# Kernel optimization log

Measured on AMD Instinct MI355X. Metric: run time of the kernel, lower is better.

## Reference

```python
import jax, jax.numpy as jnp
import numpy as np
import math

WINDOW = 512
N_HEAD = 16

def setup_inputs() -> dict:
    key = jax.random.key(0)
    ks = jax.random.split(key, 5)
    B, L, D = 2, 4096, 1024
    s = 0.02
    return {
        "x": jax.random.normal(ks[0], (B, L, D), dtype=jnp.float32),
        "Wq": jax.random.normal(ks[1], (D, D), dtype=jnp.float32) * s,
        "bq": jnp.zeros((D,), jnp.float32),
        "Wk": jax.random.normal(ks[2], (D, D), dtype=jnp.float32) * s,
        "bk": jnp.zeros((D,), jnp.float32),
        "Wv": jax.random.normal(ks[3], (D, D), dtype=jnp.float32) * s,
        "bv": jnp.zeros((D,), jnp.float32),
        "Wo": jax.random.normal(ks[4], (D, D), dtype=jnp.float32) * s,
        "bo": jnp.zeros((D,), jnp.float32),
    }

def reference(x, Wq, bq, Wk, bk, Wv, bv, Wo, bo):
    # Chunked sliding-window MHA (eval mode, dropout inactive).
    B, L, D = x.shape
    W, H = WINDOW, N_HEAD
    dh = D // H
    C = L // W  # number of query chunks
    scale = 1.0 / math.sqrt(dh)

    # Project full sequence once (linear, per-token -> identical math).
    q = x @ Wq.T + bq
    k = x @ Wk.T + bk
    v = x @ Wv.T + bv

    # Pad K/V by one window at the front so every chunk sees 2W keys.
    kp = jnp.pad(k, ((0, 0), (W, 0), (0, 0)))
    vp = jnp.pad(v, ((0, 0), (W, 0), (0, 0)))
    idx = jnp.arange(C)[:, None] * W + jnp.arange(2 * W)[None, :]  # [C, 2W] into padded seq
    kc = kp[:, idx].reshape(B, C, 2 * W, H, dh)
    vc = vp[:, idx].reshape(B, C, 2 * W, H, dh)
    qc = q.reshape(B, C, W, H, dh)

    scores = jnp.einsum('bcqhd,bckhd->bchqk', qc, kc) * scale  # [B,C,H,W,2W]
    valid = (idx >= W)  # padded positions (chunk 0's lookback) are invalid
    scores = jnp.where(valid[None, :, None, None, :], scores, jnp.float32(-1e9))
    attn = jax.nn.softmax(scores, axis=-1)
    out = jnp.einsum('bchqk,bckhd->bcqhd', attn, vc).reshape(B, L, D)
    return out @ Wo.T + bo
```

## Files before the change

kernel.cpp:

```cpp
#include <hip/hip_runtime.h>
#include <hip/hip_bf16.h>

typedef __hip_bfloat16 bf16;
typedef __attribute__((ext_vector_type(8))) short bf16x8;
typedef __attribute__((ext_vector_type(4))) float f32x4;
typedef unsigned int u32;
typedef unsigned short u16;

#define MFMA(a,b,c) __builtin_amdgcn_mfma_f32_16x16x32_bf16((a),(b),(c),0,0,0)

__device__ __forceinline__ u16 f32_to_bf16_rtne(float f) {
  u32 b = __builtin_bit_cast(u32, f);
  b += 0x7FFFu + ((b >> 16) & 1u);
  return (u16)(b >> 16);
}
__device__ __forceinline__ float bf16_to_f32(u16 h) {
  return __builtin_bit_cast(float, (u32)h << 16);
}
__device__ __forceinline__ u32 pk2bf(float a, float b) {
  u32 ua = __builtin_bit_cast(u32, a); ua += 0x7FFFu + ((ua >> 16) & 1u);
  u32 ub = __builtin_bit_cast(u32, b); ub += 0x7FFFu + ((ub >> 16) & 1u);
  return __builtin_amdgcn_perm(ub, ua, 0x07060302u);
}

__device__ __forceinline__ void gload_lds16(const bf16* g, bf16* l) {
  __builtin_amdgcn_global_load_lds(
      (const __attribute__((address_space(1))) u32*)g,
      (__attribute__((address_space(3))) u32*)l, 16, 0, 0);
}

__device__ __forceinline__ void barrier_lgkm() {
  asm volatile("s_waitcnt lgkmcnt(0)\n\ts_barrier" ::: "memory");
}

static constexpr float SL2E = 0.125f * 1.44269504f;

__global__ void detect_mode(const u16* __restrict__ x_raw, int* __restrict__ flag) {
  __shared__ int cnt;
  if (threadIdx.x == 0) cnt = 0;
  __syncthreads();
  int ok = 0;
  for (int i = threadIdx.x; i < 1024; i += 256) {
    const int e = (x_raw[2 * i] >> 7) & 0xFF;
    if (e >= 117 && e <= 137) ok++;
  }
  atomicAdd(&cnt, ok);
  __syncthreads();
  if (threadIdx.x == 0) *flag = (cnt < 512) ? 1 : 0;
}

__device__ __forceinline__ void cast8(const void* src, u16* dst, int mode, size_t i) {
  union { u16 h[8]; uint4 v; } u;
  if (mode) {
    const float4* s = (const float4*)src + i * 2;
    const float4 a = s[0], b = s[1];
    u.h[0] = f32_to_bf16_rtne(a.x); u.h[1] = f32_to_bf16_rtne(a.y);
    u.h[2] = f32_to_bf16_rtne(a.z); u.h[3] = f32_to_bf16_rtne(a.w);
    u.h[4] = f32_to_bf16_rtne(b.x); u.h[5] = f32_to_bf16_rtne(b.y);
    u.h[6] = f32_to_bf16_rtne(b.z); u.h[7] = f32_to_bf16_rtne(b.w);
  } else {
    u.v = ((const uint4*)src)[i];
  }
  ((uint4*)dst)[i] = u.v;
}

__global__ __launch_bounds__(256)
void cast_x_kernel(const void* __restrict__ src, u16* __restrict__ dst,
                   const int* __restrict__ flag, int n8) {
  const int i = blockIdx.x * 256 + threadIdx.x;
  if (i < n8) cast8(src, dst, *flag, (size_t)i);
}

__global__ __launch_bounds__(256)
void cast_w4_kernel(const void* __restrict__ wq, const void* __restrict__ wk,
                    const void* __restrict__ wv, const void* __restrict__ wo,
                    u16* __restrict__ wqkv, u16* __restrict__ wob,
                    const int* __restrict__ flag) {
  const size_t DD8 = (size_t)1024 * 1024 / 8;
  const int m = blockIdx.x >> 9;
  const size_t i = ((size_t)(blockIdx.x & 511)) * 256 + threadIdx.x;
  const void* src = (m == 0) ? wq : (m == 1) ? wk : (m == 2) ? wv : wo;
  u16* dst = (m < 3) ? (wqkv + (size_t)m * DD8 * 8) : wob;
  cast8(src, dst, *flag, i);
}

template <int MODE>
__global__ __launch_bounds__(256)
void gemm_bt(const bf16* __restrict__ A, const bf16* __restrict__ W,
             const void* __restrict__ b0, const void* __restrict__ b1,
             const void* __restrict__ b2, void* __restrict__ o0,
             void* __restrict__ o1, void* __restrict__ o2,
             const int* __restrict__ flag, int M, int N, int K)
{
  constexpr int BM = 128, BN = 128, BK = 64;
  __shared__ bf16 As[BM * BK];
  __shared__ bf16 Bs[BN * BK];

  const int mode = *flag;
  const int tid  = threadIdx.x;
  const int wave = tid >> 6, lane = tid & 63;
  const int quad = lane >> 4, l16 = lane & 15;
  const int wm   = wave >> 1, wn  = wave & 1;
  const int m0   = blockIdx.x * BM, n0 = blockIdx.y * BN;

  const int band = n0 >> 10;
  const void* bias = (band == 0) ? b0 : (band == 1) ? b1 : b2;

  const int lrow = lane >> 3;
  const int lcol = (lane & 7) * 8;

  f32x4 acc[4][4] = {};

  for (int k0 = 0; k0 < K; k0 += BK) {
    __syncthreads();
#pragma unroll
    for (int it = 0; it < 4; ++it) {
      const int rb = wave * 32 + it * 8;
      gload_lds16(A + (size_t)(m0 + rb + lrow) * K + k0 + lcol, As + rb * BK);
      gload_lds16(W + (size_t)(n0 + rb + lrow) * K + k0 + lcol, Bs + rb * BK);
    }
    __syncthreads();
#pragma unroll
    for (int kk = 0; kk < BK; kk += 32) {
      bf16x8 af[4], bw[4];
#pragma unroll
      for (int mt = 0; mt < 4; ++mt)
        af[mt] = *(const bf16x8*)(As + (wm * 64 + mt * 16 + l16) * BK + kk + quad * 8);
#pragma unroll
      for (int nt = 0; nt < 4; ++nt)
        bw[nt] = *(const bf16x8*)(Bs + (wn * 64 + nt * 16 + l16) * BK + kk + quad * 8);
#pragma unroll
      for (int mt = 0; mt < 4; ++mt)
#pragma unroll
        for (int nt = 0; nt < 4; ++nt)
          acc[mt][nt] = MFMA(af[mt], bw[nt], acc[mt][nt]);
    }
  }

#pragma unroll
  for (int nt = 0; nt < 4; ++nt) {
    const int col = n0 + wn * 64 + nt * 16 + l16;
    const int cl  = col & 1023;
    const float bv = mode ? ((const float*)bias)[cl]
                          : bf16_to_f32(((const u16*)bias)[cl]);
#pragma unroll
    for (int mt = 0; mt < 4; ++mt) {
      const int rbase = m0 + wm * 64 + mt * 16 + quad * 4;
      if (MODE == 1) {
#pragma unroll
        for (int r = 0; r < 4; ++r) {
          const float val = acc[mt][nt][r] + bv;
          const size_t idx = (size_t)(rbase + r) * N + col;
          if (mode) ((float*)o0)[idx] = val;
          else      ((u16*)o0)[idx]   = f32_to_bf16_rtne(val);
        }
      } else if (band == 2) {
        const int hh = cl >> 6, dd = cl & 63;
        const int bb = rbase >> 12, tl = rbase & 4095;
        u16* dst = (u16*)o2 + ((size_t)((bb * 16 + hh) * 64 + dd)) * 4096 + tl;
        uint2 pk;
        pk.x = pk2bf(acc[mt][nt][0] + bv, acc[mt][nt][1] + bv);
        pk.y = pk2bf(acc[mt][nt][2] + bv, acc[mt][nt][3] + bv);
        *(uint2*)dst = pk;
      } else {
        u16* dst = (u16*)((band == 0) ? o0 : o1);
        const float sc = (band == 0) ? SL2E : 1.0f;
#pragma unroll
        for (int r = 0; r < 4; ++r)
          dst[(size_t)(rbase + r) * 1024 + cl] =
              f32_to_bf16_rtne((acc[mt][nt][r] + bv) * sc);
      }
    }
  }
}

__global__ __launch_bounds__(256)
void attn_swin(const bf16* __restrict__ qb, const bf16* __restrict__ kb,
               const bf16* __restrict__ vtb, u16* __restrict__ ctx)
{
  __shared__ __align__(16) bf16 Ks[64 * 72];
  __shared__ __align__(16) bf16 Vts[64 * 72];

  int bid = blockIdx.x;
  const int g  = bid & 255, qt = bid >> 8;
  const int h  = g & 15, c = (g >> 4) & 7, b = g >> 7;

  const int tid  = threadIdx.x;
  const int w    = tid >> 6, lane = tid & 63;
  const int quad = lane >> 4, l16 = lane & 15;

  const int tq0  = c * 512 + qt * 128;
  const int hoff = h * 64;
  const int kstart = (c == 0) ? 0 : (c - 1) * 512;
  const int nkt    = (c == 0) ? 8 : 16;

  bf16x8 qf[2][2];
#pragma unroll
  for (int u = 0; u < 2; ++u) {
    const bf16* qr = qb + ((size_t)(b * 4096 + tq0 + w * 32 + u * 16 + l16)) * 1024 + hoff;
    qf[u][0] = *(const bf16x8*)(qr + quad * 8);
    qf[u][1] = *(const bf16x8*)(qr + 32 + quad * 8);
  }

  const int m    = tid >> 2;
  const int cseg = (tid & 3) * 16;
  const int sig  = (((m >> 4) & 1) << 5) | (((m >> 2) & 3) << 3)
                 | (((m >> 5) & 1) << 2) | (m & 3);
  const bf16* kgp = kb + ((size_t)(b * 4096 + kstart + sig)) * 1024 + hoff + cseg;
  const bf16* vgp = vtb + ((size_t)((b * 16 + h) * 64 + m)) * 4096 + kstart + cseg;
  bf16* kdst = Ks  + m * 72 + cseg;
  bf16* vdst = Vts + m * 72 + cseg;

  float l_i[2] = {0.f, 0.f};
  f32x4 o[2][4] = {};

  uint4 ka0 = *(const uint4*)(kgp), ka1 = *(const uint4*)(kgp + 8);
  uint4 va0 = *(const uint4*)(vgp), va1 = *(const uint4*)(vgp + 8);
  kgp += (size_t)64 * 1024; vgp += 64;

  for (int t = 0; t < nkt; ++t) {
    uint4 kb0, kb1, vb0, vb1;
    if (t + 1 < nkt) {
      kb0 = *(const uint4*)(kgp); kb1 = *(const uint4*)(kgp + 8);
      vb0 = *(const uint4*)(vgp); vb1 = *(const uint4*)(vgp + 8);
      kgp += (size_t)64 * 1024; vgp += 64;
    }
    *(uint4*)(kdst) = ka0; *(uint4*)(kdst + 8) = ka1;
    *(uint4*)(vdst) = va0; *(uint4*)(vdst + 8) = va1;
    barrier_lgkm();

    f32x4 s[2][4] = {};
#pragma unroll
    for (int kt = 0; kt < 4; ++kt) {
      const bf16* kr = Ks + (kt * 16 + l16) * 72;
      bf16x8 kf0 = *(const bf16x8*)(kr + quad * 8);
      bf16x8 kf1 = *(const bf16x8*)(kr + 32 + quad * 8);
      s[0][kt] = MFMA(kf0, qf[0][0], s[0][kt]);
      s[0][kt] = MFMA(kf1, qf[0][1], s[0][kt]);
      s[1][kt] = MFMA(kf0, qf[1][0], s[1][kt]);
      s[1][kt] = MFMA(kf1, qf[1][1], s[1][kt]);
    }

    typedef union { u32 d[4]; bf16x8 v; } fragu;
    fragu pf[2][2];
#pragma unroll
    for (int u = 0; u < 2; ++u) {
      float rs = 0.f;
#pragma unroll
      for (int kt = 0; kt < 4; ++kt)
#pragma unroll
        for (int r = 0; r < 4; ++r) {
          const float p = __builtin_amdgcn_exp2f(s[u][kt][r]);
          s[u][kt][r] = p;
          rs += p;
        }
      rs += __shfl_xor(rs, 16);
      rs += __shfl_xor(rs, 32);
      l_i[u] += rs;
#pragma unroll
      for (int hh = 0; hh < 2; ++hh)
#pragma unroll
        for (int dw = 0; dw < 4; ++dw) {
          const int kt = 2 * (dw >> 1) + hh, r0 = 2 * (dw & 1);
          pf[u][hh].d[dw] = pk2bf(s[u][kt][r0], s[u][kt][r0 + 1]);
        }
    }

#pragma unroll
    for (int dt = 0; dt < 4; ++dt) {
      const bf16* vr = Vts + (dt * 16 + l16) * 72;
      bf16x8 vf0 = *(const bf16x8*)(vr + quad * 8);
      bf16x8 vf1 = *(const bf16x8*)(vr + 32 + quad * 8);
      o[0][dt] = MFMA(vf0, pf[0][0].v, o[0][dt]);
      o[0][dt] = MFMA(vf1, pf[0][1].v, o[0][dt]);
      o[1][dt] = MFMA(vf0, pf[1][0].v, o[1][dt]);
      o[1][dt] = MFMA(vf1, pf[1][1].v, o[1][dt]);
    }
    barrier_lgkm();

    ka0 = kb0; ka1 = kb1; va0 = vb0; va1 = vb1;
  }

#pragma unroll
  for (int u = 0; u < 2; ++u) {
    const float inv = 1.0f / l_i[u];
    const int qrow = tq0 + w * 32 + u * 16 + l16;
    u16* crow = ctx + ((size_t)(b * 4096 + qrow)) * 1024 + hoff;
#pragma unroll
    for (int dt = 0; dt < 4; ++dt) {
      uint2 pk;
      pk.x = pk2bf(o[u][dt][0] * inv, o[u][dt][1] * inv);
      pk.y = pk2bf(o[u][dt][2] * inv, o[u][dt][3] * inv);
      *(uint2*)(crow + dt * 16 + quad * 4) = pk;
    }
  }
}

extern "C" void kernel_launch(void* const* d_in, const int* in_sizes, int n_in,
                              void* d_out, int out_size, void* d_ws, size_t ws_size,
                              hipStream_t stream) {
  const void* x  = d_in[0];
  const void* Wq = d_in[1];
  const void* bq = d_in[2];
  const void* Wk = d_in[3];
  const void* bk = d_in[4];
  const void* Wv = d_in[5];
  const void* bv = d_in[6];
  const void* Wo = d_in[7];
  const void* bo = d_in[8];

  const size_t MD = (size_t)8192 * 1024;
  const size_t DD = (size_t)1024 * 1024;

  char* ws = (char*)d_ws;
  int*  flag  = (int*)ws;                     ws += 256;
  u16*  xb    = (u16*)ws;                     ws += MD * 2;
  u16*  Wqkvb = (u16*)ws;                     ws += 3 * DD * 2;
  u16*  Wob   = (u16*)ws;                     ws += DD * 2;
  u16*  qbuf  = (u16*)ws;                     ws += MD * 2;
  u16*  kbuf  = (u16*)ws;                     ws += MD * 2;
  u16*  vtb   = (u16*)ws;                     ws += MD * 2;
  u16*  ctx   = (u16*)ws;

  detect_mode<<<dim3(1), dim3(256), 0, stream>>>((const u16*)x, flag);
  cast_x_kernel<<<dim3(4096), dim3(256), 0, stream>>>(x, xb, flag, (int)(MD / 8));
  cast_w4_kernel<<<dim3(2048), dim3(256), 0, stream>>>(Wq, Wk, Wv, Wo, Wqkvb, Wob, flag);

  gemm_bt<0><<<dim3(64, 24), dim3(256), 0, stream>>>(
      (const bf16*)xb, (const bf16*)Wqkvb, bq, bk, bv,
      qbuf, kbuf, vtb, flag, 8192, 3072, 1024);

  attn_swin<<<dim3(1024), dim3(256), 0, stream>>>(
      (const bf16*)qbuf, (const bf16*)kbuf, (const bf16*)vtb, ctx);

  gemm_bt<1><<<dim3(64, 8), dim3(256), 0, stream>>>(
      (const bf16*)ctx, (const bf16*)Wob, bo, bo, bo,
      d_out, nullptr, nullptr, flag, 8192, 1024, 1024);
}
```

Measured before the change: 282.5 us.

## Register-prefetch GEMM tiles with XOR-swizzled LDS and merge cast kernels

The GEMM no longer uses direct global-to-LDS loads. It prefetches the next K tile into registers while the current tile is computed, then writes it into LDS with an XOR swizzle meant to avoid bank conflicts on the MFMA fragment reads. The separate x and weight cast kernels are merged into one launch to save launch overhead. The swizzle and register double buffer add register pressure and an extra store pass through VGPRs.

```diff
diff --git a/kernel.cpp b/kernel.cpp
--- a/kernel.cpp
+++ b/kernel.cpp
@@ -21,12 +21,6 @@
   u32 ua = __builtin_bit_cast(u32, a); ua += 0x7FFFu + ((ua >> 16) & 1u);
   u32 ub = __builtin_bit_cast(u32, b); ub += 0x7FFFu + ((ub >> 16) & 1u);
   return __builtin_amdgcn_perm(ub, ua, 0x07060302u);
-}
-
-__device__ __forceinline__ void gload_lds16(const bf16* g, bf16* l) {
-  __builtin_amdgcn_global_load_lds(
-      (const __attribute__((address_space(1))) u32*)g,
-      (__attribute__((address_space(3))) u32*)l, 16, 0, 0);
 }
 
 __device__ __forceinline__ void barrier_lgkm() {
@@ -65,23 +59,23 @@
 }
 
 __global__ __launch_bounds__(256)
-void cast_x_kernel(const void* __restrict__ src, u16* __restrict__ dst,
-                   const int* __restrict__ flag, int n8) {
-  const int i = blockIdx.x * 256 + threadIdx.x;
-  if (i < n8) cast8(src, dst, *flag, (size_t)i);
-}
-
-__global__ __launch_bounds__(256)
-void cast_w4_kernel(const void* __restrict__ wq, const void* __restrict__ wk,
-                    const void* __restrict__ wv, const void* __restrict__ wo,
-                    u16* __restrict__ wqkv, u16* __restrict__ wob,
-                    const int* __restrict__ flag) {
-  const size_t DD8 = (size_t)1024 * 1024 / 8;
-  const int m = blockIdx.x >> 9;
-  const size_t i = ((size_t)(blockIdx.x & 511)) * 256 + threadIdx.x;
-  const void* src = (m == 0) ? wq : (m == 1) ? wk : (m == 2) ? wv : wo;
-  u16* dst = (m < 3) ? (wqkv + (size_t)m * DD8 * 8) : wob;
-  cast8(src, dst, *flag, i);
+void cast_all(const void* __restrict__ x,
+              const void* __restrict__ wq, const void* __restrict__ wk,
+              const void* __restrict__ wv, const void* __restrict__ wo,
+              u16* __restrict__ xb, u16* __restrict__ wqkv,
+              u16* __restrict__ wob, const int* __restrict__ flag) {
+  const int mode = *flag;
+  const int bid = blockIdx.x;
+  if (bid < 4096) {
+    cast8(x, xb, mode, (size_t)bid * 256 + threadIdx.x);
+  } else {
+    const size_t DD8 = (size_t)1024 * 1024 / 8;
+    const int m = (bid - 4096) >> 9;
+    const size_t i = ((size_t)((bid - 4096) & 511)) * 256 + threadIdx.x;
+    const void* src = (m == 0) ? wq : (m == 1) ? wk : (m == 2) ? wv : wo;
+    u16* dst = (m < 3) ? (wqkv + (size_t)m * DD8 * 8) : wob;
+    cast8(src, dst, mode, i);
+  }
 }
 
 template <int MODE>
@@ -92,43 +86,70 @@
              void* __restrict__ o1, void* __restrict__ o2,
              const int* __restrict__ flag, int M, int N, int K)
 {
-  constexpr int BM = 128, BN = 128, BK = 64;
-  __shared__ bf16 As[BM * BK];
-  __shared__ bf16 Bs[BN * BK];
+  __shared__ bf16 As[128 * 64];
+  __shared__ bf16 Bs[128 * 64];
 
   const int mode = *flag;
   const int tid  = threadIdx.x;
   const int wave = tid >> 6, lane = tid & 63;
   const int quad = lane >> 4, l16 = lane & 15;
   const int wm   = wave >> 1, wn  = wave & 1;
-  const int m0   = blockIdx.x * BM, n0 = blockIdx.y * BN;
+  const int m0   = blockIdx.x * 128, n0 = blockIdx.y * 128;
 
   const int band = n0 >> 10;
   const void* bias = (band == 0) ? b0 : (band == 1) ? b1 : b2;
 
-  const int lrow = lane >> 3;
-  const int lcol = (lane & 7) * 8;
+  const int srow = lane >> 3;
+  const int sg   = lane & 7;
+  const bf16* aSrc = A + (size_t)(m0 + wave * 32 + srow) * K + sg * 8;
+  const bf16* wSrc = W + (size_t)(n0 + wave * 32 + srow) * K + sg * 8;
+  bf16* aDst = As + (wave * 32 + srow) * 64 + ((sg ^ srow) * 8);
+  bf16* wDst = Bs + (wave * 32 + srow) * 64 + ((sg ^ srow) * 8);
+
+  const int niter = K >> 6;
+  uint4 ra[2][4], rb[2][4];
+#pragma unroll
+  for (int i = 0; i < 4; ++i) {
+    ra[0][i] = *(const uint4*)(aSrc + (size_t)i * 8 * K);
+    rb[0][i] = *(const uint4*)(wSrc + (size_t)i * 8 * K);
+  }
+  aSrc += 64; wSrc += 64;
 
   f32x4 acc[4][4] = {};
 
-  for (int k0 = 0; k0 < K; k0 += BK) {
-    __syncthreads();
-#pragma unroll
-    for (int it = 0; it < 4; ++it) {
-      const int rb = wave * 32 + it * 8;
-      gload_lds16(A + (size_t)(m0 + rb + lrow) * K + k0 + lcol, As + rb * BK);
-      gload_lds16(W + (size_t)(n0 + rb + lrow) * K + k0 + lcol, Bs + rb * BK);
-    }
-    __syncthreads();
-#pragma unroll
-    for (int kk = 0; kk < BK; kk += 32) {
+  const int arow[4] = { (wm * 64 + 0 * 16 + l16) * 64, (wm * 64 + 1 * 16 + l16) * 64,
+                        (wm * 64 + 2 * 16 + l16) * 64, (wm * 64 + 3 * 16 + l16) * 64 };
+  const int brow[4] = { (wn * 64 + 0 * 16 + l16) * 64, (wn * 64 + 1 * 16 + l16) * 64,
+                        (wn * 64 + 2 * 16 + l16) * 64, (wn * 64 + 3 * 16 + l16) * 64 };
+  const int r7 = l16 & 7;
+
+#pragma unroll 2
+  for (int t = 0; t < niter; ++t) {
+    const int cur = t & 1, nxt = cur ^ 1;
+    if (t) barrier_lgkm();
+#pragma unroll
+    for (int i = 0; i < 4; ++i) {
+      *(uint4*)(aDst + i * 512) = ra[cur][i];
+      *(uint4*)(wDst + i * 512) = rb[cur][i];
+    }
+    barrier_lgkm();
+    if (t + 1 < niter) {
+#pragma unroll
+      for (int i = 0; i < 4; ++i) {
+        ra[nxt][i] = *(const uint4*)(aSrc + (size_t)i * 8 * K);
+        rb[nxt][i] = *(const uint4*)(wSrc + (size_t)i * 8 * K);
+      }
+      aSrc += 64; wSrc += 64;
+    }
+#pragma unroll
+    for (int kk = 0; kk < 2; ++kk) {
       bf16x8 af[4], bw[4];
 #pragma unroll
       for (int mt = 0; mt < 4; ++mt)
-        af[mt] = *(const bf16x8*)(As + (wm * 64 + mt * 16 + l16) * BK + kk + quad * 8);
+        af[mt] = *(const bf16x8*)(As + arow[mt] + (((kk * 4 + quad) ^ r7) * 8));
 #pragma unroll
       for (int nt = 0; nt < 4; ++nt)
-        bw[nt] = *(const bf16x8*)(Bs + (wn * 64 + nt * 16 + l16) * BK + kk + quad * 8);
+        bw[nt] = *(const bf16x8*)(Bs + brow[nt] + (((kk * 4 + quad) ^ r7) * 8));
 #pragma unroll
       for (int mt = 0; mt < 4; ++mt)
 #pragma unroll
@@ -323,8 +344,8 @@
   u16*  ctx   = (u16*)ws;
 
   detect_mode<<<dim3(1), dim3(256), 0, stream>>>((const u16*)x, flag);
-  cast_x_kernel<<<dim3(4096), dim3(256), 0, stream>>>(x, xb, flag, (int)(MD / 8));
-  cast_w4_kernel<<<dim3(2048), dim3(256), 0, stream>>>(Wq, Wk, Wv, Wo, Wqkvb, Wob, flag);
+  cast_all<<<dim3(6144), dim3(256), 0, stream>>>(x, Wq, Wk, Wv, Wo,
+                                                 xb, Wqkvb, Wob, flag);
 
   gemm_bt<0><<<dim3(64, 24), dim3(256), 0, stream>>>(
       (const bf16*)xb, (const bf16*)Wqkvb, bq, bk, bv,
```

After: 499.5 us. +76.8%, slower.
